# Kernel optimization log

Hardware: AMD Instinct MI355X
Metric: run time of the kernel (lower is better)

The kernel has to match this reference:

```python
import jax, jax.numpy as jnp
import numpy as np
from jax import lax

CONF_THRESH = 0.65
NMS_THRESH = 0.55
EPS = 1e-16


def setup_inputs() -> dict:
    key = jax.random.key(0)
    x = jax.random.uniform(key, (8, 4096, 85), dtype=jnp.float32)
    return {"x": x}


def _xywh2xyxy(b):
    # b: [..., 4] center-x, center-y, w, h -> x1, y1, x2, y2
    cx, cy, w, h = b[..., 0], b[..., 1], b[..., 2], b[..., 3]
    return jnp.stack([cx - w / 2, cy - h / 2, cx + w / 2, cy + h / 2], axis=-1)


def _pairwise_iou(boxes):
    # boxes: [bs, N, 4] in xyxy -> iou: [bs, N, N]
    x1, y1, x2, y2 = boxes[..., 0], boxes[..., 1], boxes[..., 2], boxes[..., 3]
    ix1 = jnp.maximum(x1[:, :, None], x1[:, None, :])
    iy1 = jnp.maximum(y1[:, :, None], y1[:, None, :])
    ix2 = jnp.minimum(x2[:, :, None], x2[:, None, :])
    iy2 = jnp.minimum(y2[:, :, None], y2[:, None, :])
    inter = jnp.clip(ix2 - ix1, 0.0) * jnp.clip(iy2 - iy1, 0.0)
    area = (x2 - x1) * (y2 - y1)
    return inter / (area[:, :, None] + area[:, None, :] - inter + EPS)


def reference(x):
    # x: [bs, N, 5 + nC]
    bs, N, _ = x.shape
    obj = x[..., 4]
    valid = obj > CONF_THRESH                      # foreground filter
    boxes = _xywh2xyxy(x[..., :4])
    max_conf = jnp.max(x[..., 5:], axis=-1)        # per-box best class score
    cls_idx = jnp.argmax(x[..., 5:], axis=-1)

    # sort descending by class confidence (invalid boxes pushed to the end)
    sort_key = jnp.where(valid, max_conf, -jnp.inf)
    order = jnp.argsort(-sort_key, axis=1)         # [bs, N]
    boxes_s = jnp.take_along_axis(boxes, order[..., None], axis=1)
    obj_s = jnp.take_along_axis(obj, order, axis=1)
    conf_s = jnp.take_along_axis(max_conf, order, axis=1)
    cls_s = jnp.take_along_axis(cls_idx, order, axis=1)
    valid_s = jnp.take_along_axis(valid, order, axis=1)

    # candidate suppression matrix: same class AND IoU above threshold
    iou = _pairwise_iou(boxes_s)                   # [bs, N, N]
    same_cls = cls_s[:, :, None] == cls_s[:, None, :]
    sup_mat = (iou > NMS_THRESH) & same_cls        # [bs, N, N]

    # greedy sequential NMS over boxes in descending-score order
    def step(suppressed, xs):
        sup_row, vld, i = xs                       # sup_row: [bs, N], vld: [bs]
        keep_i = vld & ~suppressed[:, i]
        suppressed = suppressed | (keep_i[:, None] & sup_row)
        return suppressed, keep_i

    xs = (jnp.swapaxes(sup_mat, 0, 1), valid_s.T, jnp.arange(N))
    _, keeps = lax.scan(step, jnp.zeros((bs, N), dtype=bool), xs)
    keep = keeps.T                                 # [bs, N]

    # [batch_idx, x1, y1, x2, y2, p_obj, max_conf, cls_idx]; non-kept rows zeroed
    batch_idx = jnp.broadcast_to(
        jnp.arange(bs, dtype=x.dtype)[:, None, None], (bs, N, 1))
    preds = jnp.concatenate(
        [batch_idx, boxes_s, obj_s[..., None], conf_s[..., None],
         cls_s[..., None].astype(x.dtype)], axis=-1)  # [bs, N, 8]
    return preds * keep[..., None].astype(x.dtype)
```

## Files before the change

kernel.cpp:

```cpp
#include <hip/hip_runtime.h>

constexpr int BS = 8;
constexpr int N  = 4096;
constexpr int F  = 85;
constexpr int NC = 80;
constexpr float CONF_T = 0.65f;
constexpr float NMS_T  = 0.55f;
constexpr int MC   = 96;
constexpr int SEGR = 32;
constexpr int SEGS = N / SEGR;


__global__ __launch_bounds__(256) void prep_kernel(
        const float* __restrict__ x,
        unsigned long long* __restrict__ gkeys,
        float4* __restrict__ vbox,
        float2* __restrict__ vco,
        int* __restrict__ cntblk,
        float4* __restrict__ out) {
    __shared__ __align__(16) float sx[SEGR * F];
    __shared__ int wq[4];
    const int tid = threadIdx.x, blk = blockIdx.x;
    const int row0 = blk * SEGR;
    const int b = blk >> 7;
    const float4* src = (const float4*)(x + (size_t)row0 * F);
    float4* dst = (float4*)sx;
    constexpr int NV4 = SEGR * F / 4;
    for (int i = tid; i < NV4; i += 256) dst[i] = src[i];
    if (tid < SEGR * 2)
        out[(size_t)row0 * 2 + tid] = make_float4(0.f, 0.f, 0.f, 0.f);
    __syncthreads();

    const int r = tid >> 3, h = tid & 7;
    float best; int bidx;
    {
        const float* p = sx + r * F + 5 + h * 10;
        float bv = p[0]; int bi = 0;
        #pragma unroll
        for (int c = 1; c < 10; ++c) {
            float v = p[c];
            if (v > bv) { bv = v; bi = c; }
        }
        best = bv; bidx = bi + h * 10;
    }
    #pragma unroll
    for (int d = 1; d < 8; d <<= 1) {
        float ov = __shfl_xor(best, d);
        int   oi = __shfl_xor(bidx, d);
        if (ov > best || (ov == best && oi < bidx)) { best = ov; bidx = oi; }
    }

    bool valid = false;
    unsigned long long key = 0;
    if (h == 0) {
        const float* p = sx + r * F;
        float obj = p[4];
        valid = obj > CONF_T;
        const int t = row0 + r;
        if (valid) {
            float cx = p[0], cy = p[1], w = p[2], hh = p[3];
            vbox[t] = make_float4(cx - w * 0.5f, cy - hh * 0.5f,
                                  cx + w * 0.5f, cy + hh * 0.5f);
            vco[t]  = make_float2(obj, best);
            key = ((unsigned long long)(~__float_as_uint(best)) << 19)
                | ((unsigned long long)(unsigned)(t & (N - 1)) << 7)
                | (unsigned)bidx;
        }
    }
    const int lane = tid & 63, w = tid >> 6;
    unsigned long long mask = __ballot(valid);
    if (lane == 0) wq[w] = __popcll(mask);
    __syncthreads();
    int base = 0;
    for (int i = 0; i < w; ++i) base += wq[i];
    if (valid) {
        int slot = base + __popcll(mask & ((1ull << lane) - 1ull));
        gkeys[((size_t)b << 12) + ((blk & (SEGS - 1)) << 5) + slot] = key;
    }
    if (tid == 0) cntblk[blk] = wq[0] + wq[1] + wq[2] + wq[3];
}

__global__ __launch_bounds__(256) void cnms_kernel(
        const unsigned long long* __restrict__ gkeys,
        const float4* __restrict__ vbox,
        const float2* __restrict__ vco,
        const int* __restrict__ cntblk,
        float4* __restrict__ out) {
    __shared__ __align__(16) unsigned long long sk[N + 130];
    __shared__ int scnt[SEGS];
    __shared__ int soff[SEGS];
    __shared__ int snv, sm;
    __shared__ unsigned long long skm[MC];
    __shared__ int2 spart[256];
    __shared__ float4 sbox[MC];
    __shared__ float2 sco[MC];
    __shared__ int sgrk[MC];
    __shared__ unsigned char srem[MC];
    const int c = blockIdx.x, b = blockIdx.y, tid = threadIdx.x;
    const int bN = b << 12;
    const int li = tid & 63, q = tid >> 6;

    const unsigned long long* kb = gkeys + ((size_t)b << 12);
    const ulonglong2* kb2 = (const ulonglong2*)kb;
    ulonglong2 v[8];
    #pragma unroll
    for (int r = 0; r < 8; ++r) v[r] = kb2[tid + r * 256];

    if (tid < 64) {
        int v0 = cntblk[b * SEGS + 2 * tid];
        int v1 = cntblk[b * SEGS + 2 * tid + 1];
        int s = v0 + v1;
        int xx = s;
        #pragma unroll
        for (int d = 1; d < 64; d <<= 1) {
            int y = __shfl_up(xx, d);
            if (tid >= d) xx += y;
        }
        int excl = xx - s;
        scnt[2 * tid] = v0;  scnt[2 * tid + 1] = v1;
        soff[2 * tid] = excl; soff[2 * tid + 1] = excl + v0;
        if (tid == 63) snv = xx;
    }
    __syncthreads();
    const int nv = snv;

    #pragma unroll
    for (int r = 0; r < 8; ++r) {
        int s0 = (tid + r * 256) << 1;
        int s = s0 >> 5, j = s0 & 31;
        int cn = scnt[s], of = soff[s];
        if (j < cn)     sk[of + j]     = v[r].x;
        if (j + 1 < cn) sk[of + j + 1] = v[r].y;
    }
    if (tid == 0) { sk[nv] = ~0ull; sk[nv + 1] = ~0ull; }
    __syncthreads();

    if (tid < 64) {
        int mcount = 0;
        const int nch = (nv + 127) >> 7;
        for (int rc = 0; rc < nch; ++rc) {
            int j0i = (rc << 7) + tid;
            unsigned long long k0 = sk[j0i];
            unsigned long long k1 = sk[j0i + 64];
            bool m0 = (j0i < nv)      && ((int)(k0 & 127u) == c);
            bool m1 = (j0i + 64 < nv) && ((int)(k1 & 127u) == c);
            unsigned long long mb0 = __ballot(m0);
            unsigned long long mb1 = __ballot(m1);
            if (m0) {
                int pos = mcount + __popcll(mb0 & ((1ull << tid) - 1ull));
                if (pos < MC) skm[pos] = k0;
            }
            int n0 = __popcll(mb0);
            if (m1) {
                int pos = mcount + n0 + __popcll(mb1 & ((1ull << tid) - 1ull));
                if (pos < MC) skm[pos] = k1;
            }
            mcount += n0 + __popcll(mb1);
        }
        if (tid == 0) sm = (mcount < MC) ? mcount : MC;
    }
    __syncthreads();
    const int m = sm;
    if (m == 0) return;

    const unsigned long long mk0 = (li < m)      ? skm[li]      : ~0ull;
    const unsigned long long mk1 = (64 + li < m) ? skm[64 + li] : ~0ull;
    const int P = (nv + 1) >> 1;
    const int j0 = (P * q) >> 2, j1 = (P * (q + 1)) >> 2;
    const ulonglong2* skp = (const ulonglong2*)sk;
    int cr0 = 0, cr1 = 0;
    if (m > 64) {
        for (int j = j0; j < j1; ++j) {
            ulonglong2 kk = skp[j];
            cr0 += (kk.x < mk0) + (kk.y < mk0);
            cr1 += (kk.x < mk1) + (kk.y < mk1);
        }
    } else {
        for (int j = j0; j < j1; ++j) {
            ulonglong2 kk = skp[j];
            cr0 += (kk.x < mk0) + (kk.y < mk0);
        }
    }
    spart[tid] = make_int2(cr0, cr1);
    __syncthreads();

    if (tid < 64) {
        if (li < m) {
            int grk = spart[li].x + spart[64 + li].x
                    + spart[128 + li].x + spart[192 + li].x;
            int wrk = 0;
            for (int i2 = 0; i2 < m; ++i2) wrk += (skm[i2] < mk0);
            int idx = (int)((mk0 >> 7) & (N - 1));
            sbox[wrk] = vbox[bN + idx];
            sco[wrk]  = vco[bN + idx];
            sgrk[wrk] = grk;
            srem[wrk] = 0;
        }
        if (m > 64 && 64 + li < m) {
            int grk = spart[li].y + spart[64 + li].y
                    + spart[128 + li].y + spart[192 + li].y;
            int wrk = 0;
            for (int i2 = 0; i2 < m; ++i2) wrk += (skm[i2] < mk1);
            int idx = (int)((mk1 >> 7) & (N - 1));
            sbox[wrk] = vbox[bN + idx];
            sco[wrk]  = vco[bN + idx];
            sgrk[wrk] = grk;
            srem[wrk] = 0;
        }
        for (int i = 0; i < m; ++i) {
            if (srem[i]) continue;
            float4 bi4 = sbox[i];
            float ai = (bi4.z - bi4.x) * (bi4.w - bi4.y);
            for (int j = i + 1 + li; j < m; j += 64) {
                if (!srem[j]) {
                    float4 bj = sbox[j];
                    float ix1 = fmaxf(bi4.x, bj.x);
                    float iy1 = fmaxf(bi4.y, bj.y);
                    float ix2 = fminf(bi4.z, bj.z);
                    float iy2 = fminf(bi4.w, bj.w);
                    float inter = fmaxf(ix2 - ix1, 0.0f) * fmaxf(iy2 - iy1, 0.0f);
                    float aj = (bj.z - bj.x) * (bj.w - bj.y);
                    float iou = inter / (ai + aj - inter + 1e-16f);
                    if (iou > NMS_T) srem[j] = 1;
                }
            }
        }
        for (int j = li; j < m; j += 64) {
            if (!srem[j]) {
                float4 bq = sbox[j];
                float2 oc = sco[j];
                float4* o = out + (size_t)(bN + sgrk[j]) * 2;
                o[0] = make_float4((float)b, bq.x, bq.y, bq.z);
                o[1] = make_float4(bq.w, oc.x, oc.y, (float)c);
            }
        }
    }
}

extern "C" void kernel_launch(void* const* d_in, const int* in_sizes, int n_in,
                              void* d_out, int out_size, void* d_ws, size_t ws_size,
                              hipStream_t stream) {
    const float* x = (const float*)d_in[0];
    float4* out = (float4*)d_out;

    char* ws = (char*)d_ws;
    size_t off = 0;
    auto alloc = [&](size_t bytes) { char* p = ws + off; off += (bytes + 255) & ~255ull; return p; };
    unsigned long long* gkeys = (unsigned long long*)alloc(BS * N * 8);
    float4* vbox = (float4*)alloc(BS * N * 16);
    float2* vco  = (float2*)alloc(BS * N * 8);
    int*    cntblk = (int*)alloc(BS * SEGS * 4);

    prep_kernel<<<BS * N / SEGR, 256, 0, stream>>>(x, gkeys, vbox, vco, cntblk, out);
    cnms_kernel<<<dim3(NC, BS), 256, 0, stream>>>(gkeys, vbox, vco, cntblk, out);
}
```

Before: 85.44 us.

## Fuse prep and per-class NMS into one launch with flag-based inter-block sync

Result: slower. 111.0 us (+29.9%).

```diff
diff --git a/kernel.cpp b/kernel.cpp
--- a/kernel.cpp
+++ b/kernel.cpp
@@ -9,106 +9,126 @@
 constexpr int MC   = 96;
 constexpr int SEGR = 32;
 constexpr int SEGS = N / SEGR;
-
-
-__global__ __launch_bounds__(256) void prep_kernel(
+constexpr int PREP_BLKS = BS * SEGS;
+constexpr int CNMS_BLKS = NC * BS;
+constexpr unsigned TAG   = 0xAB130000u;
+
+
+struct SmemP {
+    float sx[SEGR * F];
+    int wq[4];
+};
+struct SmemC {
+    unsigned long long sk[N + 130];
+    int scnt[SEGS];
+    int soff[SEGS];
+    int snv, smm;
+    unsigned long long skm[MC];
+    int2 spart[256];
+    float4 sbox[MC];
+    float2 sco[MC];
+    int sgrk[MC];
+    unsigned char srem[MC];
+};
+
+__global__ __launch_bounds__(256) void fused_kernel(
         const float* __restrict__ x,
         unsigned long long* __restrict__ gkeys,
         float4* __restrict__ vbox,
         float2* __restrict__ vco,
-        int* __restrict__ cntblk,
+        unsigned* __restrict__ cntblk,
         float4* __restrict__ out) {
-    __shared__ __align__(16) float sx[SEGR * F];
-    __shared__ int wq[4];
+    __shared__ __align__(16) union USm { SmemP p; SmemC c; } sm;
     const int tid = threadIdx.x, blk = blockIdx.x;
-    const int row0 = blk * SEGR;
-    const int b = blk >> 7;
-    const float4* src = (const float4*)(x + (size_t)row0 * F);
-    float4* dst = (float4*)sx;
-    constexpr int NV4 = SEGR * F / 4;
-    for (int i = tid; i < NV4; i += 256) dst[i] = src[i];
-    if (tid < SEGR * 2)
-        out[(size_t)row0 * 2 + tid] = make_float4(0.f, 0.f, 0.f, 0.f);
-    __syncthreads();
-
-    const int r = tid >> 3, h = tid & 7;
-    float best; int bidx;
-    {
-        const float* p = sx + r * F + 5 + h * 10;
-        float bv = p[0]; int bi = 0;
+
+    if (blk < PREP_BLKS) {
+        const int row0 = blk * SEGR;
+        const int b = blk >> 7;
+        const float4* src = (const float4*)(x + (size_t)row0 * F);
+        float4* dst = (float4*)sm.p.sx;
+        constexpr int NV4 = SEGR * F / 4;
+        for (int i = tid; i < NV4; i += 256) dst[i] = src[i];
+        if (tid < SEGR * 2)
+            out[(size_t)row0 * 2 + tid] = make_float4(0.f, 0.f, 0.f, 0.f);
+        __syncthreads();
+
+        const int r = tid >> 3, h = tid & 7;
+        float best; int bidx;
+        {
+            const float* p = sm.p.sx + r * F + 5 + h * 10;
+            float bv = p[0]; int bi = 0;
+            #pragma unroll
+            for (int c = 1; c < 10; ++c) {
+                float v = p[c];
+                if (v > bv) { bv = v; bi = c; }
+            }
+            best = bv; bidx = bi + h * 10;
+        }
         #pragma unroll
-        for (int c = 1; c < 10; ++c) {
-            float v = p[c];
-            if (v > bv) { bv = v; bi = c; }
-        }
-        best = bv; bidx = bi + h * 10;
-    }
-    #pragma unroll
-    for (int d = 1; d < 8; d <<= 1) {
-        float ov = __shfl_xor(best, d);
-        int   oi = __shfl_xor(bidx, d);
-        if (ov > best || (ov == best && oi < bidx)) { best = ov; bidx = oi; }
-    }
-
-    bool valid = false;
-    unsigned long long key = 0;
-    if (h == 0) {
-        const float* p = sx + r * F;
-        float obj = p[4];
-        valid = obj > CONF_T;
-        const int t = row0 + r;
+        for (int d = 1; d < 8; d <<= 1) {
+            float ov = __shfl_xor(best, d);
+            int   oi = __shfl_xor(bidx, d);
+            if (ov > best || (ov == best && oi < bidx)) { best = ov; bidx = oi; }
+        }
+
+        bool valid = false;
+        unsigned long long key = 0;
+        if (h == 0) {
+            const float* p = sm.p.sx + r * F;
+            float obj = p[4];
+            valid = obj > CONF_T;
+            const int t = row0 + r;
+            if (valid) {
+                float cx = p[0], cy = p[1], w = p[2], hh = p[3];
+                vbox[t] = make_float4(cx - w * 0.5f, cy - hh * 0.5f,
+                                      cx + w * 0.5f, cy + hh * 0.5f);
+                vco[t]  = make_float2(obj, best);
+                key = ((unsigned long long)(~__float_as_uint(best)) << 19)
+                    | ((unsigned long long)(unsigned)(t & (N - 1)) << 7)
+                    | (unsigned)bidx;
+            }
+        }
+        const int lane = tid & 63, w = tid >> 6;
+        unsigned long long mask = __ballot(valid);
+        if (lane == 0) sm.p.wq[w] = __popcll(mask);
+        __syncthreads();
+        int base = 0;
+        for (int i = 0; i < w; ++i) base += sm.p.wq[i];
         if (valid) {
-            float cx = p[0], cy = p[1], w = p[2], hh = p[3];
-            vbox[t] = make_float4(cx - w * 0.5f, cy - hh * 0.5f,
-                                  cx + w * 0.5f, cy + hh * 0.5f);
-            vco[t]  = make_float2(obj, best);
-            key = ((unsigned long long)(~__float_as_uint(best)) << 19)
-                | ((unsigned long long)(unsigned)(t & (N - 1)) << 7)
-                | (unsigned)bidx;
-        }
-    }
-    const int lane = tid & 63, w = tid >> 6;
-    unsigned long long mask = __ballot(valid);
-    if (lane == 0) wq[w] = __popcll(mask);
-    __syncthreads();
-    int base = 0;
-    for (int i = 0; i < w; ++i) base += wq[i];
-    if (valid) {
-        int slot = base + __popcll(mask & ((1ull << lane) - 1ull));
-        gkeys[((size_t)b << 12) + ((blk & (SEGS - 1)) << 5) + slot] = key;
-    }
-    if (tid == 0) cntblk[blk] = wq[0] + wq[1] + wq[2] + wq[3];
-}
-
-__global__ __launch_bounds__(256) void cnms_kernel(
-        const unsigned long long* __restrict__ gkeys,
-        const float4* __restrict__ vbox,
-        const float2* __restrict__ vco,
-        const int* __restrict__ cntblk,
-        float4* __restrict__ out) {
-    __shared__ __align__(16) unsigned long long sk[N + 130];
-    __shared__ int scnt[SEGS];
-    __shared__ int soff[SEGS];
-    __shared__ int snv, sm;
-    __shared__ unsigned long long skm[MC];
-    __shared__ int2 spart[256];
-    __shared__ float4 sbox[MC];
-    __shared__ float2 sco[MC];
-    __shared__ int sgrk[MC];
-    __shared__ unsigned char srem[MC];
-    const int c = blockIdx.x, b = blockIdx.y, tid = threadIdx.x;
+            int slot = base + __popcll(mask & ((1ull << lane) - 1ull));
+            gkeys[((size_t)b << 12) + ((blk & (SEGS - 1)) << 5) + slot] = key;
+        }
+        __syncthreads();
+        if (tid == 0) {
+            unsigned total = (unsigned)(sm.p.wq[0] + sm.p.wq[1]
+                                      + sm.p.wq[2] + sm.p.wq[3]);
+            __hip_atomic_store(&cntblk[blk], total | TAG,
+                               __ATOMIC_RELEASE, __HIP_MEMORY_SCOPE_AGENT);
+        }
+        return;
+    }
+
+    const int blk2 = blk - PREP_BLKS;
+    const int c = blk2 % NC, b = blk2 / NC;
     const int bN = b << 12;
     const int li = tid & 63, q = tid >> 6;
 
-    const unsigned long long* kb = gkeys + ((size_t)b << 12);
-    const ulonglong2* kb2 = (const ulonglong2*)kb;
-    ulonglong2 v[8];
-    #pragma unroll
-    for (int r = 0; r < 8; ++r) v[r] = kb2[tid + r * 256];
-
     if (tid < 64) {
-        int v0 = cntblk[b * SEGS + 2 * tid];
-        int v1 = cntblk[b * SEGS + 2 * tid + 1];
+        const unsigned* cb = cntblk + b * SEGS;
+        unsigned u0, u1;
+        for (;;) {
+            u0 = __hip_atomic_load(&cb[2 * tid], __ATOMIC_ACQUIRE,
+                                   __HIP_MEMORY_SCOPE_AGENT);
+            if ((u0 & 0xFFFF0000u) == TAG) break;
+            __builtin_amdgcn_s_sleep(2);
+        }
+        for (;;) {
+            u1 = __hip_atomic_load(&cb[2 * tid + 1], __ATOMIC_ACQUIRE,
+                                   __HIP_MEMORY_SCOPE_AGENT);
+            if ((u1 & 0xFFFF0000u) == TAG) break;
+            __builtin_amdgcn_s_sleep(2);
+        }
+        int v0 = (int)(u0 & 0xFFFFu), v1 = (int)(u1 & 0xFFFFu);
         int s = v0 + v1;
         int xx = s;
         #pragma unroll
@@ -117,22 +137,25 @@
             if (tid >= d) xx += y;
         }
         int excl = xx - s;
-        scnt[2 * tid] = v0;  scnt[2 * tid + 1] = v1;
-        soff[2 * tid] = excl; soff[2 * tid + 1] = excl + v0;
-        if (tid == 63) snv = xx;
-    }
-    __syncthreads();
-    const int nv = snv;
-
+        sm.c.scnt[2 * tid] = v0;  sm.c.scnt[2 * tid + 1] = v1;
+        sm.c.soff[2 * tid] = excl; sm.c.soff[2 * tid + 1] = excl + v0;
+        if (tid == 63) sm.c.snv = xx;
+    }
+    __syncthreads();
+    const int nv = sm.c.snv;
+
+    const unsigned long long* kb = gkeys + ((size_t)b << 12);
+    const ulonglong2* kb2 = (const ulonglong2*)kb;
     #pragma unroll
     for (int r = 0; r < 8; ++r) {
+        ulonglong2 vv = kb2[tid + r * 256];
         int s0 = (tid + r * 256) << 1;
         int s = s0 >> 5, j = s0 & 31;
-        int cn = scnt[s], of = soff[s];
-        if (j < cn)     sk[of + j]     = v[r].x;
-        if (j + 1 < cn) sk[of + j + 1] = v[r].y;
-    }
-    if (tid == 0) { sk[nv] = ~0ull; sk[nv + 1] = ~0ull; }
+        int cn = sm.c.scnt[s], of = sm.c.soff[s];
+        if (j < cn)     sm.c.sk[of + j]     = vv.x;
+        if (j + 1 < cn) sm.c.sk[of + j + 1] = vv.y;
+    }
+    if (tid == 0) { sm.c.sk[nv] = ~0ull; sm.c.sk[nv + 1] = ~0ull; }
     __syncthreads();
 
     if (tid < 64) {
@@ -140,34 +163,34 @@
         const int nch = (nv + 127) >> 7;
         for (int rc = 0; rc < nch; ++rc) {
             int j0i = (rc << 7) + tid;
-            unsigned long long k0 = sk[j0i];
-            unsigned long long k1 = sk[j0i + 64];
+            unsigned long long k0 = sm.c.sk[j0i];
+            unsigned long long k1 = sm.c.sk[j0i + 64];
             bool m0 = (j0i < nv)      && ((int)(k0 & 127u) == c);
             bool m1 = (j0i + 64 < nv) && ((int)(k1 & 127u) == c);
             unsigned long long mb0 = __ballot(m0);
             unsigned long long mb1 = __ballot(m1);
             if (m0) {
                 int pos = mcount + __popcll(mb0 & ((1ull << tid) - 1ull));
-                if (pos < MC) skm[pos] = k0;
+                if (pos < MC) sm.c.skm[pos] = k0;
             }
             int n0 = __popcll(mb0);
             if (m1) {
                 int pos = mcount + n0 + __popcll(mb1 & ((1ull << tid) - 1ull));
-                if (pos < MC) skm[pos] = k1;
+                if (pos < MC) sm.c.skm[pos] = k1;
             }
             mcount += n0 + __popcll(mb1);
         }
-        if (tid == 0) sm = (mcount < MC) ? mcount : MC;
-    }
-    __syncthreads();
-    const int m = sm;
+        if (tid == 0) sm.c.smm = (mcount < MC) ? mcount : MC;
+    }
+    __syncthreads();
+    const int m = sm.c.smm;
     if (m == 0) return;
 
-    const unsigned long long mk0 = (li < m)      ? skm[li]      : ~0ull;
-    const unsigned long long mk1 = (64 + li < m) ? skm[64 + li] : ~0ull;
+    const unsigned long long mk0 = (li < m)      ? sm.c.skm[li]      : ~0ull;
+    const unsigned long long mk1 = (64 + li < m) ? sm.c.skm[64 + li] : ~0ull;
     const int P = (nv + 1) >> 1;
     const int j0 = (P * q) >> 2, j1 = (P * (q + 1)) >> 2;
-    const ulonglong2* skp = (const ulonglong2*)sk;
+    const ulonglong2* skp = (const ulonglong2*)sm.c.sk;
     int cr0 = 0, cr1 = 0;
     if (m > 64) {
         for (int j = j0; j < j1; ++j) {
@@ -181,39 +204,39 @@
             cr0 += (kk.x < mk0) + (kk.y < mk0);
         }
     }
-    spart[tid] = make_int2(cr0, cr1);
+    sm.c.spart[tid] = make_int2(cr0, cr1);
     __syncthreads();
 
     if (tid < 64) {
         if (li < m) {
-            int grk = spart[li].x + spart[64 + li].x
-                    + spart[128 + li].x + spart[192 + li].x;
+            int grk = sm.c.spart[li].x + sm.c.spart[64 + li].x
+                    + sm.c.spart[128 + li].x + sm.c.spart[192 + li].x;
             int wrk = 0;
-            for (int i2 = 0; i2 < m; ++i2) wrk += (skm[i2] < mk0);
+            for (int i2 = 0; i2 < m; ++i2) wrk += (sm.c.skm[i2] < mk0);
             int idx = (int)((mk0 >> 7) & (N - 1));
-            sbox[wrk] = vbox[bN + idx];
-            sco[wrk]  = vco[bN + idx];
-            sgrk[wrk] = grk;
-            srem[wrk] = 0;
+            sm.c.sbox[wrk] = vbox[bN + idx];
+            sm.c.sco[wrk]  = vco[bN + idx];
+            sm.c.sgrk[wrk] = grk;
+            sm.c.srem[wrk] = 0;
         }
         if (m > 64 && 64 + li < m) {
-            int grk = spart[li].y + spart[64 + li].y
-                    + spart[128 + li].y + spart[192 + li].y;
+            int grk = sm.c.spart[li].y + sm.c.spart[64 + li].y
+                    + sm.c.spart[128 + li].y + sm.c.spart[192 + li].y;
             int wrk = 0;
-            for (int i2 = 0; i2 < m; ++i2) wrk += (skm[i2] < mk1);
+            for (int i2 = 0; i2 < m; ++i2) wrk += (sm.c.skm[i2] < mk1);
             int idx = (int)((mk1 >> 7) & (N - 1));
-            sbox[wrk] = vbox[bN + idx];
-            sco[wrk]  = vco[bN + idx];
-            sgrk[wrk] = grk;
-            srem[wrk] = 0;
+            sm.c.sbox[wrk] = vbox[bN + idx];
+            sm.c.sco[wrk]  = vco[bN + idx];
+            sm.c.sgrk[wrk] = grk;
+            sm.c.srem[wrk] = 0;
         }
         for (int i = 0; i < m; ++i) {
-            if (srem[i]) continue;
-            float4 bi4 = sbox[i];
+            if (sm.c.srem[i]) continue;
+            float4 bi4 = sm.c.sbox[i];
             float ai = (bi4.z - bi4.x) * (bi4.w - bi4.y);
             for (int j = i + 1 + li; j < m; j += 64) {
-                if (!srem[j]) {
-                    float4 bj = sbox[j];
+                if (!sm.c.srem[j]) {
+                    float4 bj = sm.c.sbox[j];
                     float ix1 = fmaxf(bi4.x, bj.x);
                     float iy1 = fmaxf(bi4.y, bj.y);
                     float ix2 = fminf(bi4.z, bj.z);
@@ -221,15 +244,15 @@
                     float inter = fmaxf(ix2 - ix1, 0.0f) * fmaxf(iy2 - iy1, 0.0f);
                     float aj = (bj.z - bj.x) * (bj.w - bj.y);
                     float iou = inter / (ai + aj - inter + 1e-16f);
-                    if (iou > NMS_T) srem[j] = 1;
+                    if (iou > NMS_T) sm.c.srem[j] = 1;
                 }
             }
         }
         for (int j = li; j < m; j += 64) {
-            if (!srem[j]) {
-                float4 bq = sbox[j];
-                float2 oc = sco[j];
-                float4* o = out + (size_t)(bN + sgrk[j]) * 2;
+            if (!sm.c.srem[j]) {
+                float4 bq = sm.c.sbox[j];
+                float2 oc = sm.c.sco[j];
+                float4* o = out + (size_t)(bN + sm.c.sgrk[j]) * 2;
                 o[0] = make_float4((float)b, bq.x, bq.y, bq.z);
                 o[1] = make_float4(bq.w, oc.x, oc.y, (float)c);
             }
@@ -249,8 +272,8 @@
     unsigned long long* gkeys = (unsigned long long*)alloc(BS * N * 8);
     float4* vbox = (float4*)alloc(BS * N * 16);
     float2* vco  = (float2*)alloc(BS * N * 8);
-    int*    cntblk = (int*)alloc(BS * SEGS * 4);
-
-    prep_kernel<<<BS * N / SEGR, 256, 0, stream>>>(x, gkeys, vbox, vco, cntblk, out);
-    cnms_kernel<<<dim3(NC, BS), 256, 0, stream>>>(gkeys, vbox, vco, cntblk, out);
+    unsigned* cntblk = (unsigned*)alloc(BS * SEGS * 4);
+
+    fused_kernel<<<PREP_BLKS + CNMS_BLKS, 256, 0, stream>>>(
+        x, gkeys, vbox, vco, cntblk, out);
 }
```
